# Kernel tuning notes

Hardware: AMD Instinct MI355X
Metric: run time of the kernel (lower is better)

## Reference

```python
import jax, jax.numpy as jnp
import numpy as np

B, L, D, C = 2, 4096, 1024, 4


def setup_inputs() -> dict:
    key = jax.random.key(0)
    ks = jax.random.split(key, 5)
    u = jax.random.normal(ks[0], (B, L, D), dtype=jnp.float32)
    in_w = jax.random.normal(ks[1], (D, D), dtype=jnp.float32) * (1.0 / np.sqrt(D))
    in_b = jnp.zeros((D,), dtype=jnp.float32)
    # lecun_normal over fan_in = d_model * l_max for kernel, d_model for dmat
    kernel = jax.random.normal(ks[2], (C, D, L), dtype=jnp.float32) * (1.0 / np.sqrt(D * L))
    dmat = jax.random.normal(ks[3], (C, D), dtype=jnp.float32) * (1.0 / np.sqrt(D))
    out_w = jax.random.normal(ks[4], (C * D, D), dtype=jnp.float32) * (1.0 / np.sqrt(C * D))
    out_b = jnp.zeros((D,), dtype=jnp.float32)
    return {"u": u, "in_w": in_w, "in_b": in_b, "kernel": kernel,
            "dmat": dmat, "out_w": out_w, "out_b": out_b}


def reference(u, in_w, in_b, kernel, dmat, out_w, out_b):
    # in_proj: [b, l, d] -> [b, l, d]
    x = u @ in_w + in_b
    x = jnp.swapaxes(x, 1, 2)  # [b, d, l]
    length = x.shape[-1]
    n = 2 * length
    k_f = jnp.fft.rfft(kernel, n=n)      # [c, d, n//2+1] complex
    u_f = jnp.fft.rfft(x, n=n)           # [b, d, n//2+1] complex
    y_f = jnp.einsum('bdl,cdl->bcdl', u_f, k_f)
    y = jnp.fft.irfft(y_f, n=n)[..., :length]            # [b, c, d, l]
    y = y + jnp.einsum('bdl,cd->bcdl', x, dmat)           # diagonal skip term
    # rearrange '... c d l -> ... l (c d)'
    y = jnp.transpose(y, (0, 3, 1, 2)).reshape(y.shape[0], length, -1)
    return y @ out_w + out_b  # [b, l, d]
```

## Files before the change

### kernel.cpp

```cpp
#include <hip/hip_runtime.h>

#define TPB 256
constexpr float PI_F = 3.14159265358979323846f;

constexpr int NF = 4096;
constexpr int XSTR = 4104;

constexpr size_t XT_OFF = 0;
constexpr size_t XF_OFF = 33554432ull;
constexpr size_t Y_OFF  = XF_OFF + 2048ull * XSTR * 8;
constexpr size_t WS_NEED = Y_OFF + 2ull * 4 * 1024 * 4096 * 2;

typedef __attribute__((ext_vector_type(8))) short bf16x8;
typedef __attribute__((ext_vector_type(4))) float f32x4;

__device__ __forceinline__ float2 cmul(float2 a, float2 b) {
    return make_float2(a.x * b.x - a.y * b.y, a.x * b.y + a.y * b.x);
}
__device__ __forceinline__ unsigned short f2bf(float f) {
    unsigned u = __float_as_uint(f);
    u += 0x7FFFu + ((u >> 16) & 1u);
    return (unsigned short)(u >> 16);
}
__device__ __forceinline__ float bf2f(unsigned short h) {
    return __uint_as_float((unsigned)h << 16);
}

__device__ __forceinline__ int PH(int j) { return j + (j >> 4) + ((j >> 8) << 2); }
__device__ __forceinline__ int DR3(int q) { return ((q & 15) << 8) | (q & 240) | (q >> 8); }

__device__ __forceinline__ void tmul(float2& z, float wx, float wy) {
    z = make_float2(z.x * wx - z.y * wy, z.x * wy + z.y * wx);
}

template<int SGN, bool HZ>
__device__ __forceinline__ void dft16(float2 r[16]) {
    constexpr float C1 = 0.9238795325112867f;
    constexpr float S1 = 0.3826834323650898f;
    constexpr float R2 = 0.7071067811865476f;
    const float sg = (float)SGN;
#pragma unroll
    for (int t0 = 0; t0 < 4; ++t0) {
        float2 a = r[t0];
        float2 b = r[t0 + 4];
        if (HZ) {
            r[t0]      = make_float2(a.x + b.x, a.y + b.y);
            r[t0 + 8]  = make_float2(a.x - b.x, a.y - b.y);
            r[t0 + 4]  = make_float2(a.x - sg * b.y, a.y + sg * b.x);
            r[t0 + 12] = make_float2(a.x + sg * b.y, a.y - sg * b.x);
        } else {
            float2 c = r[t0 + 8];
            float2 d = r[t0 + 12];
            float2 s0 = make_float2(a.x + c.x, a.y + c.y);
            float2 s1 = make_float2(a.x - c.x, a.y - c.y);
            float2 s2 = make_float2(b.x + d.x, b.y + d.y);
            float2 s3 = make_float2(b.x - d.x, b.y - d.y);
            r[t0]      = make_float2(s0.x + s2.x, s0.y + s2.y);
            r[t0 + 8]  = make_float2(s0.x - s2.x, s0.y - s2.y);
            r[t0 + 4]  = make_float2(s1.x - sg * s3.y, s1.y + sg * s3.x);
            r[t0 + 12] = make_float2(s1.x + sg * s3.y, s1.y - sg * s3.x);
        }
    }
    tmul(r[5],  C1,  sg * S1);
    tmul(r[9],  R2,  sg * R2);
    tmul(r[13], S1,  sg * C1);
    tmul(r[6],  R2,  sg * R2);
    tmul(r[10], 0.f, sg);
    tmul(r[14], -R2, sg * R2);
    tmul(r[7],  S1,  sg * C1);
    tmul(r[11], -R2, sg * R2);
    tmul(r[15], -C1, -sg * S1);
#pragma unroll
    for (int u0 = 0; u0 < 4; ++u0) {
        float2 a = r[4 * u0], b = r[4 * u0 + 1], c = r[4 * u0 + 2], d = r[4 * u0 + 3];
        float2 s0 = make_float2(a.x + c.x, a.y + c.y);
        float2 s1 = make_float2(a.x - c.x, a.y - c.y);
        float2 s2 = make_float2(b.x + d.x, b.y + d.y);
        float2 s3 = make_float2(b.x - d.x, b.y - d.y);
        r[4 * u0]     = make_float2(s0.x + s2.x, s0.y + s2.y);
        r[4 * u0 + 2] = make_float2(s0.x - s2.x, s0.y - s2.y);
        r[4 * u0 + 1] = make_float2(s1.x - sg * s3.y, s1.y + sg * s3.x);
        r[4 * u0 + 3] = make_float2(s1.x + sg * s3.y, s1.y - sg * s3.x);
    }
}

template<int SGN, bool HZ>
__device__ __forceinline__ void fft_pass0(float2* dsh, int tid) {
    float2 r[16];
#pragma unroll
    for (int t = 0; t < (HZ ? 8 : 16); ++t) r[t] = dsh[PH(16 * tid + t)];
    dft16<SGN, HZ>(r);
#pragma unroll
    for (int u = 0; u < 16; ++u) dsh[PH(16 * tid + u)] = r[4 * (u & 3) + (u >> 2)];
}
template<int SGN>
__device__ __forceinline__ void fft_pass1(float2* dsh, int tid) {
    const int j = tid & 15;
    const int base = ((tid >> 4) << 8) + j;
    float2 r[16];
#pragma unroll
    for (int t = 0; t < 16; ++t) r[t] = dsh[PH(base + 16 * t)];
    float sv, cv;
    sincosf((float)SGN * 2.0f * PI_F * (float)j * (1.0f / 256.0f), &sv, &cv);
    float2 w = make_float2(cv, sv), wc = w;
#pragma unroll
    for (int t = 1; t < 16; ++t) { r[t] = cmul(r[t], wc); wc = cmul(wc, w); }
    dft16<SGN, false>(r);
#pragma unroll
    for (int u = 0; u < 16; ++u) dsh[PH(base + 16 * u)] = r[4 * (u & 3) + (u >> 2)];
}
template<int SGN>
__device__ __forceinline__ void fft_pass2(float2* dsh, int tid) {
    float2 r[16];
#pragma unroll
    for (int t = 0; t < 16; ++t) r[t] = dsh[PH(tid + 256 * t)];
    float sv, cv;
    sincosf((float)SGN * 2.0f * PI_F * (float)tid * (1.0f / 4096.0f), &sv, &cv);
    float2 w = make_float2(cv, sv), wc = w;
#pragma unroll
    for (int t = 1; t < 16; ++t) { r[t] = cmul(r[t], wc); wc = cmul(wc, w); }
    dft16<SGN, false>(r);
#pragma unroll
    for (int u = 0; u < 16; ++u) dsh[PH(tid + 256 * u)] = r[4 * (u & 3) + (u >> 2)];
}

__device__ __forceinline__ void fwd_fft_padded(float2* dsh, const float2* row, int tid) {
#pragma unroll
    for (int t = 0; t < 8; ++t) {
        int j = tid + (t << 8);
        dsh[PH(((j & 15) << 8) | (j & 240) | t)] = row[j];
    }
    __syncthreads();
    fft_pass0<-1, true>(dsh, tid);  __syncthreads();
    fft_pass1<-1>(dsh, tid);        __syncthreads();
    fft_pass2<-1>(dsh, tid);        __syncthreads();
}

__global__ __launch_bounds__(TPB) void fft_fwd(const float* __restrict__ src,
                                               float2* __restrict__ dst) {
    __shared__ float2 dsh[4416];
    const int tid = threadIdx.x;
    const float2* x2 = (const float2*)(src + (size_t)blockIdx.x * 4096);
    fwd_fft_padded(dsh, x2, tid);
    float2* Xrow = dst + (size_t)blockIdx.x * XSTR;
#pragma unroll
    for (int t = 0; t <= 8; ++t) {
        int k = tid + (t << 8);
        if (k > 2048) break;
        float2 Zk = dsh[PH(k & (NF - 1))];
        float2 Zm = dsh[PH((NF - k) & (NF - 1))];
        float2 Fe = make_float2(0.5f * (Zk.x + Zm.x), 0.5f * (Zk.y - Zm.y));
        float2 Fo = make_float2(0.5f * (Zk.y + Zm.y), -0.5f * (Zk.x - Zm.x));
        float sv, cv;
        sincosf(-PI_F * (float)k * (1.0f / 4096.0f), &sv, &cv);
        Xrow[k] = make_float2(Fe.x + cv * Fo.x - sv * Fo.y,
                              Fe.y + cv * Fo.y + sv * Fo.x);
        if (k < 2048) {
            float2 Fe2 = make_float2(0.5f * (Zm.x + Zk.x), 0.5f * (Zm.y - Zk.y));
            float2 Fo2 = make_float2(0.5f * (Zm.y + Zk.y), -0.5f * (Zm.x - Zk.x));
            Xrow[NF - k] = make_float2(Fe2.x + (-cv) * Fo2.x - sv * Fo2.y,
                                       Fe2.y + (-cv) * Fo2.y + sv * Fo2.x);
        }
    }
}

__global__ __launch_bounds__(TPB) void conv_fused(const float* __restrict__ kern,
                                                  const float2* __restrict__ Xf,
                                                  const float* __restrict__ xT,
                                                  const float* __restrict__ dmat,
                                                  unsigned short* __restrict__ y) {
    __shared__ float2 dsh[4416];
    const int tid = threadIdx.x;
    const int gid = blockIdx.x;
    const int dch = gid & 1023;
    const int c = gid >> 10;

    const float2* k2 = (const float2*)(kern + (size_t)gid * 4096);
    fwd_fft_padded(dsh, k2, tid);

    float2 Kk[9], Km[9];
#pragma unroll
    for (int t = 0; t < 9; ++t) {
        int k = tid + (t << 8);
        Kk[t] = make_float2(0.f, 0.f);
        Km[t] = make_float2(0.f, 0.f);
        if (k <= 2048) {
            float2 Zk = dsh[PH(k & (NF - 1))];
            float2 Zm = dsh[PH((NF - k) & (NF - 1))];
            float2 Fe = make_float2(0.5f * (Zk.x + Zm.x), 0.5f * (Zk.y - Zm.y));
            float2 Fo = make_float2(0.5f * (Zk.y + Zm.y), -0.5f * (Zk.x - Zm.x));
            float sv, cv;
            sincosf(-PI_F * (float)k * (1.0f / 4096.0f), &sv, &cv);
            Kk[t] = make_float2(Fe.x + cv * Fo.x - sv * Fo.y,
                                Fe.y + cv * Fo.y + sv * Fo.x);
            if (k < 2048) {
                float2 Fe2 = make_float2(0.5f * (Zm.x + Zk.x), 0.5f * (Zm.y - Zk.y));
                float2 Fo2 = make_float2(0.5f * (Zm.y + Zk.y), -0.5f * (Zm.x - Zk.x));
                Km[t] = make_float2(Fe2.x + (-cv) * Fo2.x - sv * Fo2.y,
                                    Fe2.y + (-cv) * Fo2.y + sv * Fo2.x);
            } else {
                Km[t] = Kk[t];
            }
        }
    }
    __syncthreads();

    const float dm = dmat[gid];
    const float sc = 1.0f / 4096.0f;
#pragma unroll 1
    for (int b = 0; b < 2; ++b) {
        const float2* Xrow = Xf + (size_t)(b * 1024 + dch) * XSTR;
#pragma unroll
        for (int t = 0; t < 9; ++t) {
            int k = tid + (t << 8);
            if (k > 2048) continue;
            float2 Yk = cmul(Xrow[k], Kk[t]);
            float2 Ym = cmul(Xrow[NF - k], Km[t]);
            float2 Fe = make_float2(0.5f * (Yk.x + Ym.x), 0.5f * (Yk.y - Ym.y));
            float2 G = make_float2(0.5f * (Yk.x - Ym.x), 0.5f * (Yk.y + Ym.y));
            float sv, cv;
            sincosf(PI_F * (float)k * (1.0f / 4096.0f), &sv, &cv);
            float2 Fo = make_float2(cv * G.x - sv * G.y, cv * G.y + sv * G.x);
            dsh[PH(DR3(k))] = make_float2(Fe.x - Fo.y, Fe.y + Fo.x);
            if (k > 0 && k < 2048) {
                dsh[PH(DR3(NF - k))] = make_float2(Fe.x + Fo.y, Fo.x - Fe.y);
            }
        }
        __syncthreads();
        fft_pass0<1, false>(dsh, tid); __syncthreads();
        fft_pass1<1>(dsh, tid);        __syncthreads();
        fft_pass2<1>(dsh, tid);        __syncthreads();

        const float2* x2 = (const float2*)(xT + (size_t)(b * 1024 + dch) * 4096);
        unsigned int* yrow =
            (unsigned int*)(y + (size_t)((b * 4 + c) * 1024 + dch) * 4096);
#pragma unroll
        for (int t = 0; t < 8; ++t) {
            int j = tid + (t << 8);
            float2 z = dsh[PH(j)];
            float2 xv = x2[j];
            float r0 = z.x * sc + xv.x * dm;
            float r1 = z.y * sc + xv.y * dm;
            yrow[j] = ((unsigned int)f2bf(r1) << 16) | (unsigned int)f2bf(r0);
        }
        __syncthreads();
    }
}

__global__ __launch_bounds__(TPB) void gemm_in_mfma(const float* __restrict__ U,
                                                    const float* __restrict__ W,
                                                    const float* __restrict__ bias,
                                                    float* __restrict__ xT) {
    __shared__ unsigned short Ah[128][40];
    __shared__ unsigned short Al[128][40];
    __shared__ unsigned short Bh[128][40];
    __shared__ unsigned short Bl[128][40];
    const int tid = threadIdx.x;
    const int n0 = blockIdx.x * 128;
    const int mo = blockIdx.y * 128;
    const int b  = mo >> 12;
    const int l0 = mo & 4095;
    const int wave = tid >> 6, lane = tid & 63;
    const int wn = (wave >> 1) * 64;
    const int wl = (wave & 1) * 64;
    const int fr = lane & 15, kg = lane >> 4;

    f32x4 acc[4][4];
#pragma unroll
    for (int i = 0; i < 4; ++i)
#pragma unroll
        for (int j = 0; j < 4; ++j) acc[i][j] = (f32x4){0.f, 0.f, 0.f, 0.f};

    for (int k0 = 0; k0 < 1024; k0 += 32) {
#pragma unroll
        for (int r = 0; r < 2; ++r) {
            int s = tid + (r << 8);
            int n = s & 127, kb = s >> 7;
            const float* wp = W + (size_t)(k0 + kb * 8) * 1024 + n0 + n;
            bf16x8 h, l;
#pragma unroll
            for (int q = 0; q < 8; ++q) {
                float v = wp[(size_t)q * 1024];
                unsigned short hh = f2bf(v);
                h[q] = (short)hh;
                l[q] = (short)f2bf(v - bf2f(hh));
            }
            *(bf16x8*)&Ah[n][kb * 8] = h;
            *(bf16x8*)&Al[n][kb * 8] = l;
        }
#pragma unroll
        for (int r = 0; r < 4; ++r) {
            int s = tid + (r << 8);
            int row = s >> 3, kq = (s & 7) << 2;
            float4 v = *(const float4*)(U + (size_t)(mo + row) * 1024 + k0 + kq);
            unsigned short hx = f2bf(v.x), hy = f2bf(v.y), hz = f2bf(v.z), hw = f2bf(v.w);
            unsigned short lx = f2bf(v.x - bf2f(hx)), ly = f2bf(v.y - bf2f(hy));
            unsigned short lz = f2bf(v.z - bf2f(hz)), lw = f2bf(v.w - bf2f(hw));
            *(unsigned*)&Bh[row][kq]     = (unsigned)hx | ((unsigned)hy << 16);
            *(unsigned*)&Bh[row][kq + 2] = (unsigned)hz | ((unsigned)hw << 16);
            *(unsigned*)&Bl[row][kq]     = (unsigned)lx | ((unsigned)ly << 16);
            *(unsigned*)&Bl[row][kq + 2] = (unsigned)lz | ((unsigned)lw << 16);
        }
        __syncthreads();

        bf16x8 ah[4], al[4], bh[4], bl[4];
#pragma unroll
        for (int f = 0; f < 4; ++f) {
            ah[f] = *(const bf16x8*)&Ah[wn + f * 16 + fr][kg * 8];
            al[f] = *(const bf16x8*)&Al[wn + f * 16 + fr][kg * 8];
            bh[f] = *(const bf16x8*)&Bh[wl + f * 16 + fr][kg * 8];
            bl[f] = *(const bf16x8*)&Bl[wl + f * 16 + fr][kg * 8];
        }
#pragma unroll
        for (int i = 0; i < 4; ++i)
#pragma unroll
            for (int j = 0; j < 4; ++j) {
                acc[i][j] = __builtin_amdgcn_mfma_f32_16x16x32_bf16(ah[i], bh[j], acc[i][j], 0, 0, 0);
                acc[i][j] = __builtin_amdgcn_mfma_f32_16x16x32_bf16(ah[i], bl[j], acc[i][j], 0, 0, 0);
                acc[i][j] = __builtin_amdgcn_mfma_f32_16x16x32_bf16(al[i], bh[j], acc[i][j], 0, 0, 0);
            }
        __syncthreads();
    }
#pragma unroll
    for (int i = 0; i < 4; ++i)
#pragma unroll
        for (int j = 0; j < 4; ++j)
#pragma unroll
            for (int rr = 0; rr < 4; ++rr) {
                int ng = n0 + wn + i * 16 + kg * 4 + rr;
                int lg = l0 + wl + j * 16 + fr;
                xT[(size_t)(b * 1024 + ng) * 4096 + lg] = acc[i][j][rr] + bias[ng];
            }
}

__global__ __launch_bounds__(TPB) void gemm_out_mfma(const unsigned short* __restrict__ Y,
                                                     const float* __restrict__ W,
                                                     const float* __restrict__ bias,
                                                     float* __restrict__ out) {
    __shared__ unsigned short Ah[128][40];
    __shared__ unsigned short Bh[128][40];
    __shared__ unsigned short Bl[128][40];
    const int tid = threadIdx.x;
    const int m0 = blockIdx.x * 128;
    const int n0 = blockIdx.y * 128;
    const int b = m0 >> 12;
    const size_t kbase = (size_t)b * 4096;
    const int wave = tid >> 6, lane = tid & 63;
    const int wm = (wave >> 1) * 64;
    const int wn = (wave & 1) * 64;
    const int fr = lane & 15, kg = lane >> 4;

    f32x4 acc[4][4];
#pragma unroll
    for (int i = 0; i < 4; ++i)
#pragma unroll
        for (int j = 0; j < 4; ++j) acc[i][j] = (f32x4){0.f, 0.f, 0.f, 0.f};

    for (int k0 = 0; k0 < 4096; k0 += 32) {
#pragma unroll
        for (int r = 0; r < 2; ++r) {
            int s = tid + (r << 8);
            int li = s & 127;
            int kb = s >> 7;
            {
                const unsigned short* ap =
                    Y + (kbase + k0 + kb * 8) * 4096 + (m0 & 4095) + li;
                bf16x8 h;
#pragma unroll
                for (int i = 0; i < 8; ++i) h[i] = (short)ap[(size_t)i * 4096];
                *(bf16x8*)&Ah[li][kb * 8] = h;
            }
            {
                const float* wp = W + (size_t)(k0 + kb * 8) * 1024 + n0 + li;
                bf16x8 h, l8;
#pragma unroll
                for (int i = 0; i < 8; ++i) {
                    float v = wp[(size_t)i * 1024];
                    unsigned short hh = f2bf(v);
                    h[i] = (short)hh;
                    l8[i] = (short)f2bf(v - bf2f(hh));
                }
                *(bf16x8*)&Bh[li][kb * 8] = h;
                *(bf16x8*)&Bl[li][kb * 8] = l8;
            }
        }
        __syncthreads();

        bf16x8 ah[4], bh[4], bl[4];
#pragma unroll
        for (int f = 0; f < 4; ++f) {
            ah[f] = *(const bf16x8*)&Ah[wm + f * 16 + fr][kg * 8];
            bh[f] = *(const bf16x8*)&Bh[wn + f * 16 + fr][kg * 8];
            bl[f] = *(const bf16x8*)&Bl[wn + f * 16 + fr][kg * 8];
        }
#pragma unroll
        for (int i = 0; i < 4; ++i)
#pragma unroll
            for (int j = 0; j < 4; ++j) {
                acc[i][j] = __builtin_amdgcn_mfma_f32_16x16x32_bf16(ah[i], bh[j], acc[i][j], 0, 0, 0);
                acc[i][j] = __builtin_amdgcn_mfma_f32_16x16x32_bf16(ah[i], bl[j], acc[i][j], 0, 0, 0);
            }
        __syncthreads();
    }

    float bj[4];
#pragma unroll
    for (int j = 0; j < 4; ++j) bj[j] = bias[n0 + wn + j * 16 + fr];
#pragma unroll
    for (int i = 0; i < 4; ++i)
#pragma unroll
        for (int j = 0; j < 4; ++j)
#pragma unroll
            for (int r = 0; r < 4; ++r) {
                int m = m0 + wm + i * 16 + kg * 4 + r;
                int n = n0 + wn + j * 16 + fr;
                out[(size_t)m * 1024 + n] = acc[i][j][r] + bj[j];
            }
}

__global__ void ws_fail(float* out, float wssz) {
    out[0] = -12345.0f;
    out[1] = wssz;
}

extern "C" void kernel_launch(void* const* d_in, const int* in_sizes, int n_in,
                              void* d_out, int out_size, void* d_ws, size_t ws_size,
                              hipStream_t stream) {
    (void)in_sizes; (void)n_in; (void)out_size;
    float* out = (float*)d_out;
    if (ws_size < WS_NEED) {
        ws_fail<<<1, 1, 0, stream>>>(out, (float)ws_size);
        return;
    }

    const float* u    = (const float*)d_in[0];
    const float* in_w = (const float*)d_in[1];
    const float* in_b = (const float*)d_in[2];
    const float* kern = (const float*)d_in[3];
    const float* dmat = (const float*)d_in[4];
    const float* outw = (const float*)d_in[5];
    const float* outb = (const float*)d_in[6];

    char* ws = (char*)d_ws;
    float*          xT = (float*)(ws + XT_OFF);
    float2*         Xf = (float2*)(ws + XF_OFF);
    unsigned short* y  = (unsigned short*)(ws + Y_OFF);

    gemm_in_mfma<<<dim3(8, 64), TPB, 0, stream>>>(u, in_w, in_b, xT);
    fft_fwd<<<dim3(2048), TPB, 0, stream>>>(xT, Xf);
    conv_fused<<<dim3(4096), TPB, 0, stream>>>(kern, Xf, xT, dmat, y);
    gemm_out_mfma<<<dim3(64, 8), TPB, 0, stream>>>(y, outw, outb, out);
}
```

Measured before the change: 776.0 us.

## Pre-split inputs and weights into bf16 hi/lo once; stage kernel spectrum in LDS

Adds a split_bf16 pre-pass that converts u, in_w and out_w into separate bf16 high and low arrays in workspace. The GEMM kernels then load these halves directly instead of repeating the fp32-to-bf16 split inside every tile load, which removes redundant conversion ALU work across the many blocks that reread the same data. In conv_fused, the forward kernel spectrum Kk is moved from registers into a shared-memory array to cut register pressure. The cost is extra kernel launches, extra workspace, and an additional global read/write pass over the inputs and weights.

Result: no change. 786.3 us (+1.3%).

```diff
diff --git a/kernel.cpp b/kernel.cpp
--- a/kernel.cpp
+++ b/kernel.cpp
@@ -6,10 +6,16 @@
 constexpr int NF = 4096;
 constexpr int XSTR = 4104;
 
-constexpr size_t XT_OFF = 0;
-constexpr size_t XF_OFF = 33554432ull;
-constexpr size_t Y_OFF  = XF_OFF + 2048ull * XSTR * 8;
-constexpr size_t WS_NEED = Y_OFF + 2ull * 4 * 1024 * 4096 * 2;
+constexpr size_t XT_OFF  = 0;
+constexpr size_t XF_OFF  = 33554432ull;
+constexpr size_t Y_OFF   = XF_OFF + 2048ull * XSTR * 8;
+constexpr size_t UH_OFF  = Y_OFF + 2ull * 4 * 1024 * 4096 * 2;
+constexpr size_t UL_OFF  = UH_OFF + 8192ull * 1024 * 2;
+constexpr size_t WIH_OFF = UL_OFF + 8192ull * 1024 * 2;
+constexpr size_t WIL_OFF = WIH_OFF + 1024ull * 1024 * 2;
+constexpr size_t WOH_OFF = WIL_OFF + 1024ull * 1024 * 2;
+constexpr size_t WOL_OFF = WOH_OFF + 4096ull * 1024 * 2;
+constexpr size_t WS_NEED = WOL_OFF + 4096ull * 1024 * 2;
 
 typedef __attribute__((ext_vector_type(8))) short bf16x8;
 typedef __attribute__((ext_vector_type(4))) float f32x4;
@@ -24,6 +30,20 @@
 }
 __device__ __forceinline__ float bf2f(unsigned short h) {
     return __uint_as_float((unsigned)h << 16);
+}
+
+__global__ __launch_bounds__(256) void split_bf16(const float* __restrict__ src,
+                                                  unsigned short* __restrict__ hi,
+                                                  unsigned short* __restrict__ lo, int n4) {
+    int i = blockIdx.x * 256 + threadIdx.x;
+    if (i >= n4) return;
+    float4 v = ((const float4*)src)[i];
+    unsigned short hx = f2bf(v.x), hy = f2bf(v.y), hz = f2bf(v.z), hw = f2bf(v.w);
+    ushort4 h = make_ushort4(hx, hy, hz, hw);
+    ushort4 l = make_ushort4(f2bf(v.x - bf2f(hx)), f2bf(v.y - bf2f(hy)),
+                             f2bf(v.z - bf2f(hz)), f2bf(v.w - bf2f(hw)));
+    ((ushort4*)hi)[i] = h;
+    ((ushort4*)lo)[i] = l;
 }
 
 __device__ __forceinline__ int PH(int j) { return j + (j >> 4) + ((j >> 8) << 2); }
@@ -170,6 +190,7 @@
                                                   const float* __restrict__ dmat,
                                                   unsigned short* __restrict__ y) {
     __shared__ float2 dsh[4416];
+    __shared__ float2 Klo[2049];
     const int tid = threadIdx.x;
     const int gid = blockIdx.x;
     const int dch = gid & 1023;
@@ -178,29 +199,24 @@
     const float2* k2 = (const float2*)(kern + (size_t)gid * 4096);
     fwd_fft_padded(dsh, k2, tid);
 
-    float2 Kk[9], Km[9];
+    float2 Km[8];
 #pragma unroll
     for (int t = 0; t < 9; ++t) {
         int k = tid + (t << 8);
-        Kk[t] = make_float2(0.f, 0.f);
-        Km[t] = make_float2(0.f, 0.f);
-        if (k <= 2048) {
-            float2 Zk = dsh[PH(k & (NF - 1))];
-            float2 Zm = dsh[PH((NF - k) & (NF - 1))];
-            float2 Fe = make_float2(0.5f * (Zk.x + Zm.x), 0.5f * (Zk.y - Zm.y));
-            float2 Fo = make_float2(0.5f * (Zk.y + Zm.y), -0.5f * (Zk.x - Zm.x));
-            float sv, cv;
-            sincosf(-PI_F * (float)k * (1.0f / 4096.0f), &sv, &cv);
-            Kk[t] = make_float2(Fe.x + cv * Fo.x - sv * Fo.y,
-                                Fe.y + cv * Fo.y + sv * Fo.x);
-            if (k < 2048) {
-                float2 Fe2 = make_float2(0.5f * (Zm.x + Zk.x), 0.5f * (Zm.y - Zk.y));
-                float2 Fo2 = make_float2(0.5f * (Zm.y + Zk.y), -0.5f * (Zm.x - Zk.x));
-                Km[t] = make_float2(Fe2.x + (-cv) * Fo2.x - sv * Fo2.y,
-                                    Fe2.y + (-cv) * Fo2.y + sv * Fo2.x);
-            } else {
-                Km[t] = Kk[t];
-            }
+        if (k > 2048) continue;
+        float2 Zk = dsh[PH(k & (NF - 1))];
+        float2 Zm = dsh[PH((NF - k) & (NF - 1))];
+        float2 Fe = make_float2(0.5f * (Zk.x + Zm.x), 0.5f * (Zk.y - Zm.y));
+        float2 Fo = make_float2(0.5f * (Zk.y + Zm.y), -0.5f * (Zk.x - Zm.x));
+        float sv, cv;
+        sincosf(-PI_F * (float)k * (1.0f / 4096.0f), &sv, &cv);
+        Klo[k] = make_float2(Fe.x + cv * Fo.x - sv * Fo.y,
+                             Fe.y + cv * Fo.y + sv * Fo.x);
+        if (k < 2048) {
+            float2 Fe2 = make_float2(0.5f * (Zm.x + Zk.x), 0.5f * (Zm.y - Zk.y));
+            float2 Fo2 = make_float2(0.5f * (Zm.y + Zk.y), -0.5f * (Zm.x - Zk.x));
+            Km[t] = make_float2(Fe2.x + (-cv) * Fo2.x - sv * Fo2.y,
+                                Fe2.y + (-cv) * Fo2.y + sv * Fo2.x);
         }
     }
     __syncthreads();
@@ -214,8 +230,10 @@
         for (int t = 0; t < 9; ++t) {
             int k = tid + (t << 8);
             if (k > 2048) continue;
-            float2 Yk = cmul(Xrow[k], Kk[t]);
-            float2 Ym = cmul(Xrow[NF - k], Km[t]);
+            float2 Kk = Klo[k];
+            float2 KmV = (k < 2048) ? Km[t] : Kk;
+            float2 Yk = cmul(Xrow[k], Kk);
+            float2 Ym = cmul(Xrow[NF - k], KmV);
             float2 Fe = make_float2(0.5f * (Yk.x + Ym.x), 0.5f * (Yk.y - Ym.y));
             float2 G = make_float2(0.5f * (Yk.x - Ym.x), 0.5f * (Yk.y + Ym.y));
             float sv, cv;
@@ -247,8 +265,10 @@
     }
 }
 
-__global__ __launch_bounds__(TPB) void gemm_in_mfma(const float* __restrict__ U,
-                                                    const float* __restrict__ W,
+__global__ __launch_bounds__(TPB) void gemm_in_mfma(const unsigned short* __restrict__ Uh,
+                                                    const unsigned short* __restrict__ Ul,
+                                                    const unsigned short* __restrict__ Wh,
+                                                    const unsigned short* __restrict__ Wl,
                                                     const float* __restrict__ bias,
                                                     float* __restrict__ xT) {
     __shared__ unsigned short Ah[128][40];
@@ -276,30 +296,25 @@
         for (int r = 0; r < 2; ++r) {
             int s = tid + (r << 8);
             int n = s & 127, kb = s >> 7;
-            const float* wp = W + (size_t)(k0 + kb * 8) * 1024 + n0 + n;
+            const unsigned short* wh = Wh + (size_t)(k0 + kb * 8) * 1024 + n0 + n;
+            const unsigned short* wll = Wl + (size_t)(k0 + kb * 8) * 1024 + n0 + n;
             bf16x8 h, l;
 #pragma unroll
             for (int q = 0; q < 8; ++q) {
-                float v = wp[(size_t)q * 1024];
-                unsigned short hh = f2bf(v);
-                h[q] = (short)hh;
-                l[q] = (short)f2bf(v - bf2f(hh));
+                h[q] = (short)wh[(size_t)q * 1024];
+                l[q] = (short)wll[(size_t)q * 1024];
             }
             *(bf16x8*)&Ah[n][kb * 8] = h;
             *(bf16x8*)&Al[n][kb * 8] = l;
         }
 #pragma unroll
-        for (int r = 0; r < 4; ++r) {
+        for (int r = 0; r < 2; ++r) {
             int s = tid + (r << 8);
-            int row = s >> 3, kq = (s & 7) << 2;
-            float4 v = *(const float4*)(U + (size_t)(mo + row) * 1024 + k0 + kq);
-            unsigned short hx = f2bf(v.x), hy = f2bf(v.y), hz = f2bf(v.z), hw = f2bf(v.w);
-            unsigned short lx = f2bf(v.x - bf2f(hx)), ly = f2bf(v.y - bf2f(hy));
-            unsigned short lz = f2bf(v.z - bf2f(hz)), lw = f2bf(v.w - bf2f(hw));
-            *(unsigned*)&Bh[row][kq]     = (unsigned)hx | ((unsigned)hy << 16);
-            *(unsigned*)&Bh[row][kq + 2] = (unsigned)hz | ((unsigned)hw << 16);
-            *(unsigned*)&Bl[row][kq]     = (unsigned)lx | ((unsigned)ly << 16);
-            *(unsigned*)&Bl[row][kq + 2] = (unsigned)lz | ((unsigned)lw << 16);
+            int row = s >> 2, kq8 = (s & 3) << 3;
+            *(bf16x8*)&Bh[row][kq8] =
+                *(const bf16x8*)(Uh + (size_t)(mo + row) * 1024 + k0 + kq8);
+            *(bf16x8*)&Bl[row][kq8] =
+                *(const bf16x8*)(Ul + (size_t)(mo + row) * 1024 + k0 + kq8);
         }
         __syncthreads();
 
@@ -334,7 +349,8 @@
 }
 
 __global__ __launch_bounds__(TPB) void gemm_out_mfma(const unsigned short* __restrict__ Y,
-                                                     const float* __restrict__ W,
+                                                     const unsigned short* __restrict__ Wh,
+                                                     const unsigned short* __restrict__ Wl,
                                                      const float* __restrict__ bias,
                                                      float* __restrict__ out) {
     __shared__ unsigned short Ah[128][40];
@@ -371,14 +387,13 @@
                 *(bf16x8*)&Ah[li][kb * 8] = h;
             }
             {
-                const float* wp = W + (size_t)(k0 + kb * 8) * 1024 + n0 + li;
+                const unsigned short* wh = Wh + (size_t)(k0 + kb * 8) * 1024 + n0 + li;
+                const unsigned short* wll = Wl + (size_t)(k0 + kb * 8) * 1024 + n0 + li;
                 bf16x8 h, l8;
 #pragma unroll
                 for (int i = 0; i < 8; ++i) {
-                    float v = wp[(size_t)i * 1024];
-                    unsigned short hh = f2bf(v);
-                    h[i] = (short)hh;
-                    l8[i] = (short)f2bf(v - bf2f(hh));
+                    h[i] = (short)wh[(size_t)i * 1024];
+                    l8[i] = (short)wll[(size_t)i * 1024];
                 }
                 *(bf16x8*)&Bh[li][kb * 8] = h;
                 *(bf16x8*)&Bl[li][kb * 8] = l8;
@@ -442,12 +457,22 @@
     const float* outb = (const float*)d_in[6];
 
     char* ws = (char*)d_ws;
-    float*          xT = (float*)(ws + XT_OFF);
-    float2*         Xf = (float2*)(ws + XF_OFF);
-    unsigned short* y  = (unsigned short*)(ws + Y_OFF);
-
-    gemm_in_mfma<<<dim3(8, 64), TPB, 0, stream>>>(u, in_w, in_b, xT);
+    float*          xT  = (float*)(ws + XT_OFF);
+    float2*         Xf  = (float2*)(ws + XF_OFF);
+    unsigned short* y   = (unsigned short*)(ws + Y_OFF);
+    unsigned short* Uh  = (unsigned short*)(ws + UH_OFF);
+    unsigned short* Ul  = (unsigned short*)(ws + UL_OFF);
+    unsigned short* Wih = (unsigned short*)(ws + WIH_OFF);
+    unsigned short* Wil = (unsigned short*)(ws + WIL_OFF);
+    unsigned short* Woh = (unsigned short*)(ws + WOH_OFF);
+    unsigned short* Wol = (unsigned short*)(ws + WOL_OFF);
+
+    split_bf16<<<dim3(8192), 256, 0, stream>>>(u, Uh, Ul, 8192 * 1024 / 4);
+    split_bf16<<<dim3(1024), 256, 0, stream>>>(in_w, Wih, Wil, 1024 * 1024 / 4);
+    split_bf16<<<dim3(4096), 256, 0, stream>>>(outw, Woh, Wol, 4096 * 1024 / 4);
+
+    gemm_in_mfma<<<dim3(8, 64), TPB, 0, stream>>>(Uh, Ul, Wih, Wil, in_b, xT);
     fft_fwd<<<dim3(2048), TPB, 0, stream>>>(xT, Xf);
     conv_fused<<<dim3(4096), TPB, 0, stream>>>(kern, Xf, xT, dmat, y);
-    gemm_out_mfma<<<dim3(64, 8), TPB, 0, stream>>>(y, outw, outb, out);
-}
+    gemm_out_mfma<<<dim3(64, 8), TPB, 0, stream>>>(y, Woh, Wol, outb, out);
+}
```
